# Kernel tuning notes

Measured on AMD Instinct MI355X. Metric: run time of the kernel, lower is better.

Reference implementation:

```python
import jax, jax.numpy as jnp
from jax import lax
import numpy as np

B, N, E, NA = 32, 8192, 256, 16
M_MIN, M_MAX = 3, 8192
PAD_TOKEN = -2.0
LN_EPS = 1e-3  # keras LayerNormalization default epsilon


def setup_inputs() -> dict:
    key = jax.random.key(0)
    ks = jax.random.split(key, 8)
    return {
        "x": jax.random.normal(ks[0], (B, N, E), jnp.float32),
        "mask": jnp.ones((B, N), jnp.float32),
        "barcode": jax.random.uniform(ks[1], (1, 1, E), jnp.float32),
        "Wq": 0.05 * jax.random.normal(ks[2], (E, E), jnp.float32),
        "Wk": 0.05 * jax.random.normal(ks[3], (E, E), jnp.float32),
        "Wv": 0.05 * jax.random.normal(ks[4], (E, E), jnp.float32),
        "g": jax.random.uniform(ks[5], (NA, E, E), jnp.float32, minval=-0.05, maxval=0.05),
        "w": 0.05 * jax.random.normal(ks[6], (1, NA, E, E), jnp.float32),
        "ln_gamma": jnp.ones((E,), jnp.float32),
        "ln_beta": jnp.zeros((E,), jnp.float32),
    }


def _select_one(order):
    """Greedy distance-constrained selection over a descending-sorted index list (N,).
    Matches the TF while_loop: first index always kept; a candidate is kept iff its
    abs distance to every previously kept index lies in [M_MIN, M_MAX].
    Unfilled slots stay 0 (TensorArray default)."""
    slot = jnp.arange(NA, dtype=jnp.int32)

    def body(i, state):
        sel, count = state
        cand = order[i]
        d = jnp.abs(sel - cand)
        ok = (d >= M_MIN) & (d <= M_MAX)
        active = slot < count
        valid = jnp.all(jnp.where(active, ok, True)) & (count < NA)
        sel = jnp.where((slot == count) & valid, cand, sel)
        count = count + valid.astype(jnp.int32)
        return (sel, count)

    sel0 = jnp.zeros((NA,), jnp.int32).at[0].set(order[0])
    sel, _ = lax.fori_loop(1, N, body, (sel0, jnp.int32(1)))
    return sel


def reference(x, mask, barcode, Wq, Wk, Wv, g, w, ln_gamma, ln_beta):
    m = jnp.where(mask == PAD_TOKEN, 0.0, 1.0)  # (B, N)
    bc = jnp.broadcast_to(barcode, (x.shape[0], 1, x.shape[-1]))
    q = bc @ Wq              # (B, 1, E)
    k = x @ Wk               # (B, N, E)
    v = x @ Wv               # (B, N, E)
    scale = 1.0 / jnp.sqrt(jnp.float32(x.shape[-1]))
    att = jnp.einsum('bqe,bne->bqn', q, k) * scale  # (B, 1, N)
    att = att + (1.0 - m[:, None, :]) * (-1e9)
    att = jax.nn.softmax(att, axis=-1) * m[:, None, :]
    barcode_out = jnp.einsum('bqn,bne->bqe', att, v)[:, 0, :]  # (B, E)

    att1 = att[:, 0, :]                                 # (B, N)
    order = jnp.argsort(-att1, axis=-1).astype(jnp.int32)
    inds = jnp.sort(jax.vmap(_select_one)(order), axis=-1)  # (B, NA)
    weights = jnp.take_along_axis(att1, inds, axis=1)        # (B, NA)
    outs = jnp.take_along_axis(x, inds[:, :, None], axis=1)  # (B, NA, E)

    # sinusoidal positional encoding from anchor positions
    ra = jnp.arange(E, dtype=jnp.float32) / jnp.float32(E)
    pos = jnp.sin(inds[:, :, None].astype(jnp.float32) / jnp.power(40.0, ra))
    outs = outs + pos

    # per-anchor gated projection: (B,NA,1,E) @ (NA,E,E) -> (B,NA,E)
    outs_w = jnp.einsum('bae,aef->baf', outs, w[0])
    outs_g = jax.nn.sigmoid(jnp.einsum('bae,aef->baf', outs, g))
    outs = outs_w * outs_g * weights[:, :, None]

    # LayerNorm over last axis (keras defaults: eps=1e-3, learned gamma/beta)
    mu = jnp.mean(outs, axis=-1, keepdims=True)
    var = jnp.mean(jnp.square(outs - mu), axis=-1, keepdims=True)
    outs = (outs - mu) * lax.rsqrt(var + LN_EPS) * ln_gamma + ln_beta

    return (outs, inds, weights, barcode_out)
```

## Files before the change

### kernel.cpp

```cpp
#include <hip/hip_runtime.h>

#define BB 32
#define NN 8192
#define EE 256
#define NAA 16
#define NCHUNK 64
#define CHUNK 128

#define KQ_OFF   0
#define ATT_OFF  256
#define PL_OFF   (ATT_OFF + BB*NN)
#define PS_OFF   (PL_OFF + BB*NCHUNK)
#define INDS_OFF (PS_OFF + BB*NCHUNK*EE)
#define WSEL_OFF (INDS_OFF + BB*NAA)

#define OUT_OUTS 0
#define OUT_INDS (BB*NAA*EE)
#define OUT_W    (OUT_INDS + BB*NAA)
#define OUT_BC   (OUT_W + BB*NAA)

__global__ __launch_bounds__(1024) void prep_kernel(
    const float* __restrict__ barcode, const float* __restrict__ Wq,
    const float* __restrict__ Wk, float* __restrict__ ws) {
  int t = threadIdx.x & 255, q = threadIdx.x >> 8;
  __shared__ float part[4][EE];
  __shared__ float qs[EE];
  float acc = 0.f;
  #pragma unroll 8
  for (int i = 0; i < 64; ++i) {
    int f = q * 64 + i;
    acc += barcode[f] * Wq[f*EE + t];
  }
  part[q][t] = acc;
  __syncthreads();
  if (threadIdx.x < 256) qs[t] = part[0][t] + part[1][t] + part[2][t] + part[3][t];
  __syncthreads();
  const float4* wk4 = (const float4*)(Wk + (size_t)t * EE + q * 64);
  const float4* qs4 = (const float4*)(qs + q * 64);
  float acc2 = 0.f;
  #pragma unroll
  for (int i = 0; i < 16; ++i) {
    float4 wv = wk4[i], qv = qs4[i];
    acc2 += wv.x*qv.x + wv.y*qv.y + wv.z*qv.z + wv.w*qv.w;
  }
  part[q][t] = acc2;
  __syncthreads();
  if (threadIdx.x < 256)
    ws[KQ_OFF + t] = (part[0][t] + part[1][t] + part[2][t] + part[3][t]) * 0.0625f;
}

__global__ __launch_bounds__(256) void pass_a(
    const float* __restrict__ x, const float* __restrict__ mask,
    float* __restrict__ ws) {
  const int c = blockIdx.x, b = blockIdx.y;
  const int w = threadIdx.x >> 6, lane = threadIdx.x & 63;
  const float4 kq4 = ((const float4*)(ws + KQ_OFF))[lane];
  float* att = ws + ATT_OFF + (size_t)b * NN + c * CHUNK;
  const float* xb = x + ((size_t)b * NN + (size_t)c * CHUNK) * EE;
  const float* mb = mask + (size_t)b * NN + c * CHUNK;

  float l = 0.f;
  float4 acc = {0.f, 0.f, 0.f, 0.f};
  #pragma unroll 4
  for (int r = w; r < CHUNK; r += 4) {
    float4 xv = ((const float4*)(xb + (size_t)r * EE))[lane];
    float d = xv.x*kq4.x + xv.y*kq4.y + xv.z*kq4.z + xv.w*kq4.w;
    #pragma unroll
    for (int off = 32; off >= 1; off >>= 1) d += __shfl_xor(d, off, 64);
    float mk = mb[r];
    float a = d + ((mk == -2.0f) ? -1e9f : 0.0f);
    if (lane == 0) att[r] = a;
    float keep = (mk == -2.0f) ? 0.f : 1.f;
    float p = __expf(a) * keep;
    l += p;
    acc.x += p*xv.x; acc.y += p*xv.y; acc.z += p*xv.z; acc.w += p*xv.w;
  }
  __shared__ float sl[4], ss[4][EE];
  ss[w][lane*4+0] = acc.x; ss[w][lane*4+1] = acc.y;
  ss[w][lane*4+2] = acc.z; ss[w][lane*4+3] = acc.w;
  if (lane == 0) sl[w] = l;
  __syncthreads();
  int t = threadIdx.x;
  ws[PS_OFF + (size_t)(b*NCHUNK + c)*EE + t] =
      ss[0][t] + ss[1][t] + ss[2][t] + ss[3][t];
  if (t == 0) ws[PL_OFF + b*NCHUNK + c] = sl[0] + sl[1] + sl[2] + sl[3];
}

__global__ __launch_bounds__(256) void combine_select(
    const float* __restrict__ Wv, float* __restrict__ ws, float* __restrict__ out) {
  int b = blockIdx.x, t = threadIdx.x;
  int w = t >> 6, lane = t & 63;
  __shared__ float sn[EE];
  __shared__ float p[NN];
  __shared__ float wvs[4];
  __shared__ int   wis[4];
  __shared__ int   sel[NAA];
  __shared__ float selw[NAA];
  __shared__ float Lsh;
  float S = 0.f;
  for (int c = 0; c < NCHUNK; ++c)
    S += ws[PS_OFF + (size_t)(b*NCHUNK + c)*EE + t];
  if (t < 64) {
    float lv = ws[PL_OFF + b*NCHUNK + t];
    #pragma unroll
    for (int off = 32; off >= 1; off >>= 1) lv += __shfl_xor(lv, off, 64);
    if (t == 0) Lsh = lv;
  }
  __syncthreads();
  float L = Lsh;
  sn[t] = S / L;
  const float* att = ws + ATT_OFF + (size_t)b * NN;
  for (int n = t; n < NN; n += 256) p[n] = att[n];
  __syncthreads();
  float acc = 0.f;
  #pragma unroll 8
  for (int e = 0; e < EE; ++e) acc += sn[e] * Wv[e*EE + t];
  out[OUT_BC + b*EE + t] = acc;
  for (int it = 0; it < NAA; ++it) {
    float v = -INFINITY; int idx = NN;
    for (int n = t; n < NN; n += 256) {
      float pv = p[n];
      if (pv > v) { v = pv; idx = n; }
    }
    #pragma unroll
    for (int off = 32; off >= 1; off >>= 1) {
      float v2 = __shfl_xor(v, off, 64);
      int   i2 = __shfl_xor(idx, off, 64);
      if (v2 > v || (v2 == v && i2 < idx)) { v = v2; idx = i2; }
    }
    if (lane == 0) { wvs[w] = v; wis[w] = idx; }
    __syncthreads();
    if (t == 0) {
      float bvv = wvs[0]; int bii = wis[0];
      #pragma unroll
      for (int j = 1; j < 4; ++j) {
        float v2 = wvs[j]; int i2 = wis[j];
        if (v2 > bvv || (v2 == bvv && i2 < bii)) { bvv = v2; bii = i2; }
      }
      sel[it] = bii; selw[it] = bvv;
      int lo = bii - 2 < 0 ? 0 : bii - 2;
      int hi = bii + 2 > NN-1 ? NN-1 : bii + 2;
      for (int j = lo; j <= hi; ++j) p[j] = -INFINITY;
    }
    __syncthreads();
  }
  if (t == 0) {
    for (int i = 1; i < NAA; ++i) {
      int ki = sel[i]; float kw = selw[i]; int j = i - 1;
      while (j >= 0 && sel[j] > ki) { sel[j+1] = sel[j]; selw[j+1] = selw[j]; --j; }
      sel[j+1] = ki; selw[j+1] = kw;
    }
  }
  __syncthreads();
  if (t < NAA) {
    float wt = expf(selw[t]) / L;
    out[OUT_INDS + b*NAA + t] = (float)sel[t];
    out[OUT_W    + b*NAA + t] = wt;
    ((int*)(ws + INDS_OFF))[b*NAA + t] = sel[t];
    ws[WSEL_OFF + b*NAA + t] = wt;
  }
}

__global__ __launch_bounds__(256) void final_kernel(
    const float* __restrict__ x, const float* __restrict__ g,
    const float* __restrict__ w, const float* __restrict__ ln_gamma,
    const float* __restrict__ ln_beta, const float* __restrict__ ws,
    float* __restrict__ out) {
  int a = blockIdx.x, b = blockIdx.y, t = threadIdx.x;
  __shared__ float row[EE];
  __shared__ float redw[4][EE];
  __shared__ float redg[4][EE];
  __shared__ float red[4];
  int ind = ((const int*)(ws + INDS_OFF))[b*NAA + a];
  float wt = ws[WSEL_OFF + b*NAA + a];
  float ra = (float)t * (1.0f/256.0f);
  float pos = sinf((float)ind / powf(40.0f, ra));
  row[t] = x[((size_t)b * NN + ind) * EE + t] + pos;
  __syncthreads();
  int qe = t >> 6, fq = t & 63;
  const float4* wa4 = (const float4*)(w + (size_t)a * EE * EE);
  const float4* ga4 = (const float4*)(g + (size_t)a * EE * EE);
  float4 aw = {0,0,0,0}, ag = {0,0,0,0};
  #pragma unroll 8
  for (int i = 0; i < 64; ++i) {
    int e = qe * 64 + i;
    float r = row[e];
    float4 wv = wa4[(size_t)e * 64 + fq];
    float4 gv = ga4[(size_t)e * 64 + fq];
    aw.x += r*wv.x; aw.y += r*wv.y; aw.z += r*wv.z; aw.w += r*wv.w;
    ag.x += r*gv.x; ag.y += r*gv.y; ag.z += r*gv.z; ag.w += r*gv.w;
  }
  ((float4*)redw[qe])[fq] = aw;
  ((float4*)redg[qe])[fq] = ag;
  __syncthreads();
  float ow = redw[0][t] + redw[1][t] + redw[2][t] + redw[3][t];
  float og = redg[0][t] + redg[1][t] + redg[2][t] + redg[3][t];
  float val = ow * (1.f / (1.f + expf(-og))) * wt;
  int wv_ = t >> 6;
  float s = val;
  #pragma unroll
  for (int off = 32; off >= 1; off >>= 1) s += __shfl_xor(s, off, 64);
  if ((t & 63) == 0) red[wv_] = s;
  __syncthreads();
  float mu = (red[0] + red[1] + red[2] + red[3]) * (1.f/256.f);
  __syncthreads();
  float dv = val - mu, sq = dv * dv;
  #pragma unroll
  for (int off = 32; off >= 1; off >>= 1) sq += __shfl_xor(sq, off, 64);
  if ((t & 63) == 0) red[wv_] = sq;
  __syncthreads();
  float var = (red[0] + red[1] + red[2] + red[3]) * (1.f/256.f);
  out[OUT_OUTS + ((size_t)b * NAA + a) * EE + t] =
      dv * rsqrtf(var + 0.001f) * ln_gamma[t] + ln_beta[t];
}

extern "C" void kernel_launch(void* const* d_in, const int* in_sizes, int n_in,
                              void* d_out, int out_size, void* d_ws, size_t ws_size,
                              hipStream_t stream) {
  const float* x       = (const float*)d_in[0];
  const float* mask    = (const float*)d_in[1];
  const float* barcode = (const float*)d_in[2];
  const float* Wq      = (const float*)d_in[3];
  const float* Wk      = (const float*)d_in[4];
  const float* Wv      = (const float*)d_in[5];
  const float* g       = (const float*)d_in[6];
  const float* w       = (const float*)d_in[7];
  const float* gamma   = (const float*)d_in[8];
  const float* beta    = (const float*)d_in[9];
  float* out = (float*)d_out;
  float* ws  = (float*)d_ws;

  prep_kernel<<<1, 1024, 0, stream>>>(barcode, Wq, Wk, ws);
  pass_a<<<dim3(NCHUNK, BB), 256, 0, stream>>>(x, mask, ws);
  combine_select<<<BB, 256, 0, stream>>>(Wv, ws, out);
  final_kernel<<<dim3(NAA, BB), 256, 0, stream>>>(x, g, w, gamma, beta, ws, out);
}
```

Baseline: 506.9 us.

## Split prep into multi-block kernels, raise per-wave ILP in pass_a, batch final rows

The single-block prep kernel is split into two multi-block kernels: one computes q = barcode·Wq, the other computes Wk·q. This spreads the weight reads across several CUs. pass_a now has each wavefront handle four rows at once, with 16 lanes per row and four float4 loads per lane, so the cross-lane reduction is shorter and more loads are in flight. final_kernel processes four batches per block, so each w/g weight load is reused four times and weight traffic drops fourfold, at the cost of more registers and shared memory and one extra kernel launch.

```diff
diff --git a/kernel.cpp b/kernel.cpp
--- a/kernel.cpp
+++ b/kernel.cpp
@@ -13,40 +13,50 @@
 #define PS_OFF   (PL_OFF + BB*NCHUNK)
 #define INDS_OFF (PS_OFF + BB*NCHUNK*EE)
 #define WSEL_OFF (INDS_OFF + BB*NAA)
+#define Q_OFF    (WSEL_OFF + BB*NAA)
 
 #define OUT_OUTS 0
 #define OUT_INDS (BB*NAA*EE)
 #define OUT_W    (OUT_INDS + BB*NAA)
 #define OUT_BC   (OUT_W + BB*NAA)
 
-__global__ __launch_bounds__(1024) void prep_kernel(
+__global__ __launch_bounds__(256) void prep_q(
     const float* __restrict__ barcode, const float* __restrict__ Wq,
-    const float* __restrict__ Wk, float* __restrict__ ws) {
-  int t = threadIdx.x & 255, q = threadIdx.x >> 8;
-  __shared__ float part[4][EE];
-  __shared__ float qs[EE];
+    float* __restrict__ ws) {
+  int blk = blockIdx.x;
+  int cc = threadIdx.x & 63, fq = threadIdx.x >> 6;
+  int col = blk * 64 + cc;
   float acc = 0.f;
   #pragma unroll 8
   for (int i = 0; i < 64; ++i) {
-    int f = q * 64 + i;
-    acc += barcode[f] * Wq[f*EE + t];
-  }
-  part[q][t] = acc;
-  __syncthreads();
-  if (threadIdx.x < 256) qs[t] = part[0][t] + part[1][t] + part[2][t] + part[3][t];
-  __syncthreads();
-  const float4* wk4 = (const float4*)(Wk + (size_t)t * EE + q * 64);
-  const float4* qs4 = (const float4*)(qs + q * 64);
-  float acc2 = 0.f;
-  #pragma unroll
-  for (int i = 0; i < 16; ++i) {
-    float4 wv = wk4[i], qv = qs4[i];
-    acc2 += wv.x*qv.x + wv.y*qv.y + wv.z*qv.z + wv.w*qv.w;
-  }
-  part[q][t] = acc2;
-  __syncthreads();
-  if (threadIdx.x < 256)
-    ws[KQ_OFF + t] = (part[0][t] + part[1][t] + part[2][t] + part[3][t]) * 0.0625f;
+    int f = fq * 64 + i;
+    acc += barcode[f] * Wq[f * EE + col];
+  }
+  __shared__ float part[4][64];
+  part[fq][cc] = acc;
+  __syncthreads();
+  if (threadIdx.x < 64)
+    ws[Q_OFF + blk * 64 + threadIdx.x] =
+        part[0][threadIdx.x] + part[1][threadIdx.x] +
+        part[2][threadIdx.x] + part[3][threadIdx.x];
+}
+
+__global__ __launch_bounds__(256) void prep_kq(
+    const float* __restrict__ Wk, float* __restrict__ ws) {
+  int blk = blockIdx.x;
+  int fi = threadIdx.x >> 4, p = threadIdx.x & 15;
+  int f = blk * 16 + fi;
+  const float4* wk4 = (const float4*)(Wk + (size_t)f * EE);
+  const float4* q4  = (const float4*)(ws + Q_OFF);
+  float acc = 0.f;
+  #pragma unroll
+  for (int j = 0; j < 4; ++j) {
+    float4 wv = wk4[p + 16 * j], qv = q4[p + 16 * j];
+    acc += wv.x * qv.x + wv.y * qv.y + wv.z * qv.z + wv.w * qv.w;
+  }
+  #pragma unroll
+  for (int off = 8; off >= 1; off >>= 1) acc += __shfl_xor(acc, off, 64);
+  if (p == 0) ws[KQ_OFF + f] = acc * 0.0625f;
 }
 
 __global__ __launch_bounds__(256) void pass_a(
@@ -54,36 +64,56 @@
     float* __restrict__ ws) {
   const int c = blockIdx.x, b = blockIdx.y;
   const int w = threadIdx.x >> 6, lane = threadIdx.x & 63;
-  const float4 kq4 = ((const float4*)(ws + KQ_OFF))[lane];
+  const int il = lane & 15, q = lane >> 4;
+  const float4* kqp = (const float4*)(ws + KQ_OFF);
+  const float4 kq0 = kqp[il], kq1 = kqp[il + 16],
+               kq2 = kqp[il + 32], kq3 = kqp[il + 48];
   float* att = ws + ATT_OFF + (size_t)b * NN + c * CHUNK;
   const float* xb = x + ((size_t)b * NN + (size_t)c * CHUNK) * EE;
   const float* mb = mask + (size_t)b * NN + c * CHUNK;
 
   float l = 0.f;
-  float4 acc = {0.f, 0.f, 0.f, 0.f};
-  #pragma unroll 4
-  for (int r = w; r < CHUNK; r += 4) {
-    float4 xv = ((const float4*)(xb + (size_t)r * EE))[lane];
-    float d = xv.x*kq4.x + xv.y*kq4.y + xv.z*kq4.z + xv.w*kq4.w;
-    #pragma unroll
-    for (int off = 32; off >= 1; off >>= 1) d += __shfl_xor(d, off, 64);
+  float4 a0 = {0,0,0,0}, a1 = {0,0,0,0}, a2 = {0,0,0,0}, a3 = {0,0,0,0};
+  #pragma unroll
+  for (int it = 0; it < 8; ++it) {
+    int r = w * 32 + it * 4 + q;
+    const float4* xr = (const float4*)(xb + (size_t)r * EE);
+    float4 x0 = xr[il], x1 = xr[il + 16], x2 = xr[il + 32], x3 = xr[il + 48];
+    float d = x0.x*kq0.x + x0.y*kq0.y + x0.z*kq0.z + x0.w*kq0.w
+            + x1.x*kq1.x + x1.y*kq1.y + x1.z*kq1.z + x1.w*kq1.w
+            + x2.x*kq2.x + x2.y*kq2.y + x2.z*kq2.z + x2.w*kq2.w
+            + x3.x*kq3.x + x3.y*kq3.y + x3.z*kq3.z + x3.w*kq3.w;
+    d += __shfl_xor(d, 8, 64);
+    d += __shfl_xor(d, 4, 64);
+    d += __shfl_xor(d, 2, 64);
+    d += __shfl_xor(d, 1, 64);
     float mk = mb[r];
     float a = d + ((mk == -2.0f) ? -1e9f : 0.0f);
-    if (lane == 0) att[r] = a;
-    float keep = (mk == -2.0f) ? 0.f : 1.f;
-    float p = __expf(a) * keep;
+    if (il == 0) att[r] = a;
+    float p = __expf(a) * ((mk == -2.0f) ? 0.f : 1.f);
     l += p;
-    acc.x += p*xv.x; acc.y += p*xv.y; acc.z += p*xv.z; acc.w += p*xv.w;
-  }
-  __shared__ float sl[4], ss[4][EE];
-  ss[w][lane*4+0] = acc.x; ss[w][lane*4+1] = acc.y;
-  ss[w][lane*4+2] = acc.z; ss[w][lane*4+3] = acc.w;
+    a0.x += p*x0.x; a0.y += p*x0.y; a0.z += p*x0.z; a0.w += p*x0.w;
+    a1.x += p*x1.x; a1.y += p*x1.y; a1.z += p*x1.z; a1.w += p*x1.w;
+    a2.x += p*x2.x; a2.y += p*x2.y; a2.z += p*x2.z; a2.w += p*x2.w;
+    a3.x += p*x3.x; a3.y += p*x3.y; a3.z += p*x3.z; a3.w += p*x3.w;
+  }
+  __shared__ float ss[16][EE];
+  __shared__ float sl[4];
+  int s = w * 4 + q;
+  ((float4*)ss[s])[il]      = a0;
+  ((float4*)ss[s])[il + 16] = a1;
+  ((float4*)ss[s])[il + 32] = a2;
+  ((float4*)ss[s])[il + 48] = a3;
+  l += __shfl_xor(l, 16, 64);
+  l += __shfl_xor(l, 32, 64);
   if (lane == 0) sl[w] = l;
   __syncthreads();
   int t = threadIdx.x;
-  ws[PS_OFF + (size_t)(b*NCHUNK + c)*EE + t] =
-      ss[0][t] + ss[1][t] + ss[2][t] + ss[3][t];
-  if (t == 0) ws[PL_OFF + b*NCHUNK + c] = sl[0] + sl[1] + sl[2] + sl[3];
+  float S = 0.f;
+  #pragma unroll
+  for (int si = 0; si < 16; ++si) S += ss[si][t];
+  ws[PS_OFF + (size_t)(b * NCHUNK + c) * EE + t] = S;
+  if (t == 0) ws[PL_OFF + b * NCHUNK + c] = sl[0] + sl[1] + sl[2] + sl[3];
 }
 
 __global__ __launch_bounds__(256) void combine_select(
@@ -99,9 +129,9 @@
   __shared__ float Lsh;
   float S = 0.f;
   for (int c = 0; c < NCHUNK; ++c)
-    S += ws[PS_OFF + (size_t)(b*NCHUNK + c)*EE + t];
+    S += ws[PS_OFF + (size_t)(b * NCHUNK + c) * EE + t];
   if (t < 64) {
-    float lv = ws[PL_OFF + b*NCHUNK + t];
+    float lv = ws[PL_OFF + b * NCHUNK + t];
     #pragma unroll
     for (int off = 32; off >= 1; off >>= 1) lv += __shfl_xor(lv, off, 64);
     if (t == 0) Lsh = lv;
@@ -114,8 +144,8 @@
   __syncthreads();
   float acc = 0.f;
   #pragma unroll 8
-  for (int e = 0; e < EE; ++e) acc += sn[e] * Wv[e*EE + t];
-  out[OUT_BC + b*EE + t] = acc;
+  for (int e = 0; e < EE; ++e) acc += sn[e] * Wv[e * EE + t];
+  out[OUT_BC + b * EE + t] = acc;
   for (int it = 0; it < NAA; ++it) {
     float v = -INFINITY; int idx = NN;
     for (int n = t; n < NN; n += 256) {
@@ -139,7 +169,7 @@
       }
       sel[it] = bii; selw[it] = bvv;
       int lo = bii - 2 < 0 ? 0 : bii - 2;
-      int hi = bii + 2 > NN-1 ? NN-1 : bii + 2;
+      int hi = bii + 2 > NN - 1 ? NN - 1 : bii + 2;
       for (int j = lo; j <= hi; ++j) p[j] = -INFINITY;
     }
     __syncthreads();
@@ -154,10 +184,10 @@
   __syncthreads();
   if (t < NAA) {
     float wt = expf(selw[t]) / L;
-    out[OUT_INDS + b*NAA + t] = (float)sel[t];
-    out[OUT_W    + b*NAA + t] = wt;
-    ((int*)(ws + INDS_OFF))[b*NAA + t] = sel[t];
-    ws[WSEL_OFF + b*NAA + t] = wt;
+    out[OUT_INDS + b * NAA + t] = (float)sel[t];
+    out[OUT_W    + b * NAA + t] = wt;
+    ((int*)(ws + INDS_OFF))[b * NAA + t] = sel[t];
+    ws[WSEL_OFF + b * NAA + t] = wt;
   }
 }
 
@@ -166,52 +196,83 @@
     const float* __restrict__ w, const float* __restrict__ ln_gamma,
     const float* __restrict__ ln_beta, const float* __restrict__ ws,
     float* __restrict__ out) {
-  int a = blockIdx.x, b = blockIdx.y, t = threadIdx.x;
-  __shared__ float row[EE];
-  __shared__ float redw[4][EE];
-  __shared__ float redg[4][EE];
-  __shared__ float red[4];
-  int ind = ((const int*)(ws + INDS_OFF))[b*NAA + a];
-  float wt = ws[WSEL_OFF + b*NAA + a];
-  float ra = (float)t * (1.0f/256.0f);
-  float pos = sinf((float)ind / powf(40.0f, ra));
-  row[t] = x[((size_t)b * NN + ind) * EE + t] + pos;
+  int a = blockIdx.x, bg = blockIdx.y, t = threadIdx.x;
+  __shared__ float row[4][EE];
+  __shared__ float redw[4][4][EE];
+  __shared__ float redg[4][4][EE];
+  __shared__ float red[4][4];
+  float pw = powf(40.0f, (float)t * (1.0f / 256.0f));
+  float wts[4];
+  #pragma unroll
+  for (int rr = 0; rr < 4; ++rr) {
+    int b = bg * 4 + rr;
+    int ind = ((const int*)(ws + INDS_OFF))[b * NAA + a];
+    wts[rr] = ws[WSEL_OFF + b * NAA + a];
+    row[rr][t] = x[((size_t)b * NN + ind) * EE + t] + sinf((float)ind / pw);
+  }
   __syncthreads();
   int qe = t >> 6, fq = t & 63;
   const float4* wa4 = (const float4*)(w + (size_t)a * EE * EE);
   const float4* ga4 = (const float4*)(g + (size_t)a * EE * EE);
-  float4 aw = {0,0,0,0}, ag = {0,0,0,0};
-  #pragma unroll 8
+  float4 aw0={0,0,0,0}, aw1={0,0,0,0}, aw2={0,0,0,0}, aw3={0,0,0,0};
+  float4 ag0={0,0,0,0}, ag1={0,0,0,0}, ag2={0,0,0,0}, ag3={0,0,0,0};
+  #pragma unroll 4
   for (int i = 0; i < 64; ++i) {
     int e = qe * 64 + i;
-    float r = row[e];
     float4 wv = wa4[(size_t)e * 64 + fq];
     float4 gv = ga4[(size_t)e * 64 + fq];
-    aw.x += r*wv.x; aw.y += r*wv.y; aw.z += r*wv.z; aw.w += r*wv.w;
-    ag.x += r*gv.x; ag.y += r*gv.y; ag.z += r*gv.z; ag.w += r*gv.w;
-  }
-  ((float4*)redw[qe])[fq] = aw;
-  ((float4*)redg[qe])[fq] = ag;
-  __syncthreads();
-  float ow = redw[0][t] + redw[1][t] + redw[2][t] + redw[3][t];
-  float og = redg[0][t] + redg[1][t] + redg[2][t] + redg[3][t];
-  float val = ow * (1.f / (1.f + expf(-og))) * wt;
-  int wv_ = t >> 6;
-  float s = val;
-  #pragma unroll
-  for (int off = 32; off >= 1; off >>= 1) s += __shfl_xor(s, off, 64);
-  if ((t & 63) == 0) red[wv_] = s;
-  __syncthreads();
-  float mu = (red[0] + red[1] + red[2] + red[3]) * (1.f/256.f);
-  __syncthreads();
-  float dv = val - mu, sq = dv * dv;
-  #pragma unroll
-  for (int off = 32; off >= 1; off >>= 1) sq += __shfl_xor(sq, off, 64);
-  if ((t & 63) == 0) red[wv_] = sq;
-  __syncthreads();
-  float var = (red[0] + red[1] + red[2] + red[3]) * (1.f/256.f);
-  out[OUT_OUTS + ((size_t)b * NAA + a) * EE + t] =
-      dv * rsqrtf(var + 0.001f) * ln_gamma[t] + ln_beta[t];
+    float r0 = row[0][e], r1 = row[1][e], r2 = row[2][e], r3 = row[3][e];
+    aw0.x += r0*wv.x; aw0.y += r0*wv.y; aw0.z += r0*wv.z; aw0.w += r0*wv.w;
+    aw1.x += r1*wv.x; aw1.y += r1*wv.y; aw1.z += r1*wv.z; aw1.w += r1*wv.w;
+    aw2.x += r2*wv.x; aw2.y += r2*wv.y; aw2.z += r2*wv.z; aw2.w += r2*wv.w;
+    aw3.x += r3*wv.x; aw3.y += r3*wv.y; aw3.z += r3*wv.z; aw3.w += r3*wv.w;
+    ag0.x += r0*gv.x; ag0.y += r0*gv.y; ag0.z += r0*gv.z; ag0.w += r0*gv.w;
+    ag1.x += r1*gv.x; ag1.y += r1*gv.y; ag1.z += r1*gv.z; ag1.w += r1*gv.w;
+    ag2.x += r2*gv.x; ag2.y += r2*gv.y; ag2.z += r2*gv.z; ag2.w += r2*gv.w;
+    ag3.x += r3*gv.x; ag3.y += r3*gv.y; ag3.z += r3*gv.z; ag3.w += r3*gv.w;
+  }
+  ((float4*)redw[0][qe])[fq] = aw0; ((float4*)redw[1][qe])[fq] = aw1;
+  ((float4*)redw[2][qe])[fq] = aw2; ((float4*)redw[3][qe])[fq] = aw3;
+  ((float4*)redg[0][qe])[fq] = ag0; ((float4*)redg[1][qe])[fq] = ag1;
+  ((float4*)redg[2][qe])[fq] = ag2; ((float4*)redg[3][qe])[fq] = ag3;
+  __syncthreads();
+  float val[4];
+  #pragma unroll
+  for (int rr = 0; rr < 4; ++rr) {
+    float ow = redw[rr][0][t] + redw[rr][1][t] + redw[rr][2][t] + redw[rr][3][t];
+    float og = redg[rr][0][t] + redg[rr][1][t] + redg[rr][2][t] + redg[rr][3][t];
+    val[rr] = ow * (1.f / (1.f + expf(-og))) * wts[rr];
+  }
+  int wv_ = t >> 6, ln = t & 63;
+  #pragma unroll
+  for (int rr = 0; rr < 4; ++rr) {
+    float s = val[rr];
+    #pragma unroll
+    for (int off = 32; off >= 1; off >>= 1) s += __shfl_xor(s, off, 64);
+    if (ln == 0) red[rr][wv_] = s;
+  }
+  __syncthreads();
+  float mu[4], dv[4];
+  #pragma unroll
+  for (int rr = 0; rr < 4; ++rr)
+    mu[rr] = (red[rr][0] + red[rr][1] + red[rr][2] + red[rr][3]) * (1.f/256.f);
+  __syncthreads();
+  #pragma unroll
+  for (int rr = 0; rr < 4; ++rr) {
+    dv[rr] = val[rr] - mu[rr];
+    float sq = dv[rr] * dv[rr];
+    #pragma unroll
+    for (int off = 32; off >= 1; off >>= 1) sq += __shfl_xor(sq, off, 64);
+    if (ln == 0) red[rr][wv_] = sq;
+  }
+  __syncthreads();
+  #pragma unroll
+  for (int rr = 0; rr < 4; ++rr) {
+    int b = bg * 4 + rr;
+    float var = (red[rr][0] + red[rr][1] + red[rr][2] + red[rr][3]) * (1.f/256.f);
+    out[OUT_OUTS + ((size_t)b * NAA + a) * EE + t] =
+        dv[rr] * rsqrtf(var + 0.001f) * ln_gamma[t] + ln_beta[t];
+  }
 }
 
 extern "C" void kernel_launch(void* const* d_in, const int* in_sizes, int n_in,
@@ -230,8 +291,9 @@
   float* out = (float*)d_out;
   float* ws  = (float*)d_ws;
 
-  prep_kernel<<<1, 1024, 0, stream>>>(barcode, Wq, Wk, ws);
+  prep_q <<<4, 256, 0, stream>>>(barcode, Wq, ws);
+  prep_kq<<<16, 256, 0, stream>>>(Wk, ws);
   pass_a<<<dim3(NCHUNK, BB), 256, 0, stream>>>(x, mask, ws);
   combine_select<<<BB, 256, 0, stream>>>(Wv, ws, out);
-  final_kernel<<<dim3(NAA, BB), 256, 0, stream>>>(x, g, w, gamma, beta, ws, out);
-}
+  final_kernel<<<dim3(NAA, BB/4), 256, 0, stream>>>(x, g, w, gamma, beta, ws, out);
+}
```

Measured after the change: 454.9 us. 10.3% less time.
